# Kernel optimization log

Measured on AMD Instinct MI355X. Metric: run time of the kernel, lower is better.

The kernel has to match this reference:

```python
import jax, jax.numpy as jnp
import numpy as np

NA, NP = 50000, 100000  # num authors, num papers
NE = 200000             # edges per direction
H = 256


def _sage(x_src, x_dst, src, dst, Wl, bl, Wr, br, n_dst):
    # PyG SAGEConv: lin_l(mean_{j in N(i)} x_j) + lin_r(x_i)
    msg = x_src[src]                                              # [E, d_src] gather
    s = jax.ops.segment_sum(msg, dst, num_segments=n_dst)        # [n_dst, d_src]
    cnt = jax.ops.segment_sum(jnp.ones((src.shape[0],), x_src.dtype), dst, num_segments=n_dst)
    mean = s / jnp.maximum(cnt, 1.0)[:, None]
    return mean @ Wl.T + bl + x_dst @ Wr.T + br


def setup_inputs() -> dict:
    key = jax.random.key(0)
    ks = jax.random.split(key, 24)
    d = {}
    d['x_author'] = jax.random.normal(ks[0], (NA, 128), jnp.float32)
    d['x_paper'] = jax.random.normal(ks[1], (NP, 256), jnp.float32)
    src_a = jax.random.randint(ks[2], (NE,), 0, NA)
    dst_p = jax.random.randint(ks[3], (NE,), 0, NP)
    d['ei_a2p'] = jnp.stack([src_a, dst_p])                       # author -> paper
    src_p = jax.random.randint(ks[4], (NE,), 0, NP)
    dst_a = jax.random.randint(ks[5], (NE,), 0, NA)
    d['ei_p2a'] = jnp.stack([src_p, dst_a])                       # paper -> author
    sc = 0.05
    d['Wl0_ap'] = jax.random.normal(ks[6], (H, 128)) * sc
    d['bl0_ap'] = jnp.zeros((H,), jnp.float32)
    d['Wr0_ap'] = jax.random.normal(ks[7], (H, 256)) * sc
    d['br0_ap'] = jnp.zeros((H,), jnp.float32)
    d['Wl0_pa'] = jax.random.normal(ks[8], (H, 256)) * sc
    d['bl0_pa'] = jnp.zeros((H,), jnp.float32)
    d['Wr0_pa'] = jax.random.normal(ks[9], (H, 128)) * sc
    d['br0_pa'] = jnp.zeros((H,), jnp.float32)
    d['Wl_ap'] = jax.random.normal(ks[10], (2, H, H)) * sc
    d['bl_ap'] = jnp.zeros((2, H), jnp.float32)
    d['Wr_ap'] = jax.random.normal(ks[11], (2, H, H)) * sc
    d['br_ap'] = jnp.zeros((2, H), jnp.float32)
    d['Wl_pa'] = jax.random.normal(ks[12], (2, H, H)) * sc
    d['bl_pa'] = jnp.zeros((2, H), jnp.float32)
    d['Wr_pa'] = jax.random.normal(ks[13], (2, H, H)) * sc
    d['br_pa'] = jnp.zeros((2, H), jnp.float32)
    d['W_out'] = jax.random.normal(ks[14], (10, H)) * sc
    d['b_out'] = jnp.zeros((10,), jnp.float32)
    return d


def reference(x_author, x_paper, ei_a2p, ei_p2a,
              Wl0_ap, bl0_ap, Wr0_ap, br0_ap,
              Wl0_pa, bl0_pa, Wr0_pa, br0_pa,
              Wl_ap, bl_ap, Wr_ap, br_ap,
              Wl_pa, bl_pa, Wr_pa, br_pa,
              W_out, b_out):
    sa, da = ei_p2a[0], ei_p2a[1]   # paper->author edges
    sp, dp = ei_a2p[0], ei_a2p[1]   # author->paper edges
    # layer 0 (lazy dims: author 128, paper 256)
    paper = jax.nn.elu(_sage(x_author, x_paper, sp, dp, Wl0_ap, bl0_ap, Wr0_ap, br0_ap, NP))
    author = jax.nn.elu(_sage(x_paper, x_author, sa, da, Wl0_pa, bl0_pa, Wr0_pa, br0_pa, NA))
    # layers 1..2 (hidden 256)
    for l in range(2):
        new_paper = _sage(author, paper, sp, dp, Wl_ap[l], bl_ap[l], Wr_ap[l], br_ap[l], NP)
        new_author = _sage(paper, author, sa, da, Wl_pa[l], bl_pa[l], Wr_pa[l], br_pa[l], NA)
        paper = jax.nn.elu(new_paper)
        author = jax.nn.elu(new_author)
    return author @ W_out.T + b_out  # target = 'author'
```

## Files before the change

kernel.cpp:

```cpp
#include <hip/hip_runtime.h>
#include <hip/hip_bf16.h>
#include <cstddef>

#define NA 50000
#define NP 100000
#define NE 200000
#define SCAN_CHUNK 1024

typedef unsigned short u16;
typedef unsigned int u32;
typedef short v8s __attribute__((ext_vector_type(8)));
typedef float f32x4 __attribute__((ext_vector_type(4)));

__device__ __forceinline__ float elu_f(float x) {
  return x > 0.0f ? x : expm1f(x);
}
__device__ __forceinline__ u16 f2bf(float x) {
  u32 u = __float_as_uint(x);
  return (u16)((u + 0x7fffu + ((u >> 16) & 1u)) >> 16);
}
__device__ __forceinline__ float bf2f(u16 h) {
  return __uint_as_float(((u32)h) << 16);
}
__device__ __forceinline__ u32 pk2(float a, float b) {
  return (u32)f2bf(a) | ((u32)f2bf(b) << 16);
}
__device__ __forceinline__ float lo_f(u32 w) { return __uint_as_float(w << 16); }
__device__ __forceinline__ float hi_f(u32 w) { return __uint_as_float(w & 0xffff0000u); }

__device__ __forceinline__ void gload_lds16(const u16* gsrc, u16* ldst) {
  __builtin_amdgcn_global_load_lds(
      (const __attribute__((address_space(1))) u32*)gsrc,
      (__attribute__((address_space(3))) u32*)ldst, 16, 0, 0);
}

__global__ void count_deg_i(const int* __restrict__ dst_p, const int* __restrict__ dst_a,
                            int* cnt_p, int* cnt_a) {
  int i = blockIdx.x * blockDim.x + threadIdx.x;
  if (i < NE) atomicAdd(&cnt_p[dst_p[i]], 1);
  else if (i < 2 * NE) atomicAdd(&cnt_a[dst_a[i - NE]], 1);
}

__global__ void block_sums_k(const int* __restrict__ cnt, int* __restrict__ bsums, int n) {
  __shared__ int red[256];
  int t = threadIdx.x;
  int base = blockIdx.x * SCAN_CHUNK + t * 4;
  int s = 0;
  #pragma unroll
  for (int i = 0; i < 4; ++i) {
    int idx = base + i;
    if (idx < n) s += cnt[idx];
  }
  red[t] = s;
  __syncthreads();
  for (int off = 128; off > 0; off >>= 1) {
    if (t < off) red[t] += red[t + off];
    __syncthreads();
  }
  if (t == 0) bsums[blockIdx.x] = red[0];
}

__global__ void scan_bsums_k(int* bsums, int nb) {
  __shared__ int tmp[256];
  int t = threadIdx.x;
  int orig = (t < nb) ? bsums[t] : 0;
  tmp[t] = orig;
  __syncthreads();
  for (int off = 1; off < 256; off <<= 1) {
    int u = (t >= off) ? tmp[t - off] : 0;
    __syncthreads();
    tmp[t] += u;
    __syncthreads();
  }
  if (t < nb) bsums[t] = tmp[t] - orig;
}

__global__ void scan_final_k(const int* __restrict__ cnt, const int* __restrict__ bsums,
                             int* __restrict__ row_start, int* __restrict__ cursor,
                             int n, int total) {
  __shared__ int red[256];
  int t = threadIdx.x;
  int base = blockIdx.x * SCAN_CHUNK + t * 4;
  int v[4];
  int s = 0;
  #pragma unroll
  for (int i = 0; i < 4; ++i) {
    int idx = base + i;
    v[i] = (idx < n) ? cnt[idx] : 0;
    s += v[i];
  }
  int orig = s;
  red[t] = s;
  __syncthreads();
  for (int off = 1; off < 256; off <<= 1) {
    int u = (t >= off) ? red[t - off] : 0;
    __syncthreads();
    red[t] += u;
    __syncthreads();
  }
  int excl = red[t] - orig + bsums[blockIdx.x];
  #pragma unroll
  for (int i = 0; i < 4; ++i) {
    int idx = base + i;
    if (idx < n) {
      row_start[idx] = excl;
      cursor[idx] = excl;
    }
    excl += v[i];
  }
  if (blockIdx.x == 0 && t == 0) row_start[n] = total;
}

__global__ void csr_fill(const int* __restrict__ src, const int* __restrict__ dst,
                         int* cursor, int* __restrict__ csr_src) {
  int e = blockIdx.x * blockDim.x + threadIdx.x;
  if (e < NE) {
    int p = atomicAdd(&cursor[dst[e]], 1);
    csr_src[p] = src[e];
  }
}

__global__ void to_bf16(const float* __restrict__ in, u16* __restrict__ out, int n4) {
  int i = blockIdx.x * 256 + threadIdx.x;
  if (i >= n4) return;
  float4 v = ((const float4*)in)[i];
  uint2 o;
  o.x = pk2(v.x, v.y);
  o.y = pk2(v.z, v.w);
  *(uint2*)(out + (size_t)i * 4) = o;
}

struct PackJobs {
  const float* src[12];
  u16* dst[12];
  int K[12];
  int boff[13];
};

__global__ void pack_all(PackJobs J) {
  int blk = blockIdx.x;
  int j = 0;
  while (j < 11 && blk >= J.boff[j + 1]) ++j;
  int id = (blk - J.boff[j]) * 256 + threadIdx.x;
  int K = J.K[j];
  int l = id & 63;
  int c = (id >> 6) & 15;
  int ks = id >> 10;
  int n = c * 16 + (l & 15);
  int k = ks * 32 + (l >> 4) * 8;
  const float* src = J.src[j] + (size_t)n * K + k;
  uint4 o;
  o.x = pk2(src[0], src[1]);
  o.y = pk2(src[2], src[3]);
  o.z = pk2(src[4], src[5]);
  o.w = pk2(src[6], src[7]);
  *(uint4*)(J.dst[j] + (size_t)id * 8) = o;
}

struct BiasJobs {
  const float* a[6];
  const float* b[6];
  float* o[6];
};
__global__ void bias_all(BiasJobs J) {
  int j = blockIdx.x;
  int i = threadIdx.x;
  J.o[j][i] = J.a[j][i] + J.b[j][i];
}

template <int D>
__device__ __forceinline__ void gm_node(const u16* __restrict__ feat, const int* __restrict__ cs,
                                        const int* __restrict__ rs, u16* __restrict__ agg,
                                        int node, int lane) {
  int beg = rs[node], end = rs[node + 1];
  int deg = end - beg;
  if (D == 256) {
    float a0 = 0.f, a1 = 0.f, a2 = 0.f, a3 = 0.f, a4 = 0.f, a5 = 0.f, a6 = 0.f, a7 = 0.f;
    int e = beg;
    uint4 un = {0, 0, 0, 0};
    if (e < end) un = *(const uint4*)(feat + (size_t)cs[e] * 256 + lane * 8);
    while (e < end) {
      uint4 u = un;
      ++e;
      if (e < end)
        un = *(const uint4*)(feat + (size_t)cs[e] * 256 + lane * 8);
      a0 += lo_f(u.x); a1 += hi_f(u.x);
      a2 += lo_f(u.y); a3 += hi_f(u.y);
      a4 += lo_f(u.z); a5 += hi_f(u.z);
      a6 += lo_f(u.w); a7 += hi_f(u.w);
    }
    float inv = 1.0f / fmaxf((float)deg, 1.0f);
    uint4 o;
    o.x = pk2(a0 * inv, a1 * inv);
    o.y = pk2(a2 * inv, a3 * inv);
    o.z = pk2(a4 * inv, a5 * inv);
    o.w = pk2(a6 * inv, a7 * inv);
    *(uint4*)(agg + (size_t)node * 256 + lane * 8) = o;
  } else {
    float a0 = 0.f, a1 = 0.f, a2 = 0.f, a3 = 0.f;
    int e = beg;
    uint2 un = {0, 0};
    if (e < end) un = *(const uint2*)(feat + (size_t)cs[e] * 128 + lane * 4);
    while (e < end) {
      uint2 u = un;
      ++e;
      if (e < end)
        un = *(const uint2*)(feat + (size_t)cs[e] * 128 + lane * 4);
      a0 += lo_f(u.x); a1 += hi_f(u.x);
      a2 += lo_f(u.y); a3 += hi_f(u.y);
    }
    float inv = 1.0f / fmaxf((float)deg, 1.0f);
    uint2 o;
    o.x = pk2(a0 * inv, a1 * inv);
    o.y = pk2(a2 * inv, a3 * inv);
    *(uint2*)(agg + (size_t)node * 128 + lane * 4) = o;
  }
}

template <int D1, int D2>
__global__ __launch_bounds__(256) void gather2(
    const u16* __restrict__ f1, const int* __restrict__ cs1, const int* __restrict__ rs1,
    u16* __restrict__ a1, int n1,
    const u16* __restrict__ f2, const int* __restrict__ cs2, const int* __restrict__ rs2,
    u16* __restrict__ a2, int n2) {
  int hw = (blockIdx.x * 256 + threadIdx.x) >> 5;
  int lane = threadIdx.x & 31;
  if (hw < n1) gm_node<D1>(f1, cs1, rs1, a1, hw, lane);
  else if (hw - n1 < n2) gm_node<D2>(f2, cs2, rs2, a2, hw - n1, lane);
}

struct SideB {
  const u16* agg;
  const u16* x;
  const u16* Wp;
  const float* bias;
  u16* out;
  int M;
  int K1;
  int K2;
};

template <int NK>
__global__ __launch_bounds__(512, 4) void sage_pipe(SideB P, SideB A, int nbP2) {
  __shared__ __align__(16) u16 ldsw[3 * 4096];
  SideB S;
  int bid = blockIdx.x;
  if (bid < nbP2) { S = P; } else { bid -= nbP2; S = A; }
  const int cg = bid & 1;
  const int rg = bid >> 1;

  const int k1c = S.K1 >> 5;
  const int t = threadIdx.x;
  const int w = t >> 6, l = t & 63;
  const int lr = l & 15, lk = l >> 4;
  const int rowbase = rg * 256 + w * 32;

  int rowv[2];
  const u16 *pa[2], *px[2];
  #pragma unroll
  for (int rt = 0; rt < 2; ++rt) {
    int row = rowbase + rt * 16 + lr;
    rowv[rt] = row;
    int ar = min(row, S.M - 1);
    pa[rt] = S.agg + (size_t)ar * S.K1 + lk * 8;
    px[rt] = S.x + (size_t)ar * S.K2 + lk * 8;
  }

  auto xload = [&](int c, int rt) -> v8s {
    const u16* p = (c < k1c) ? (pa[rt] + c * 32) : (px[rt] + (c - k1c) * 32);
    return *(const v8s*)p;
  };
  auto wstage = [&](int c, int b) {
    const u16* gsrc = S.Wp + ((size_t)c * 1024 + cg * 512 + t) * 8;
    u16* ldst = ldsw + b * 4096 + w * 512;
    gload_lds16(gsrc, ldst);
  };

  f32x4 acc[2][8];
  #pragma unroll
  for (int rt = 0; rt < 2; ++rt)
    #pragma unroll
    for (int i = 0; i < 8; ++i) acc[rt][i] = (f32x4){0.f, 0.f, 0.f, 0.f};

  v8s xc[2], xn[2];
  xc[0] = xload(0, 0);
  xc[1] = xload(0, 1);
  wstage(0, 0);
  wstage(1, 1);
  asm volatile("s_waitcnt vmcnt(1)" ::: "memory");
  __builtin_amdgcn_s_barrier();

  #pragma unroll
  for (int s = 0; s < NK; ++s) {
    const int cur = s % 3;
    if (s + 2 < NK) wstage(s + 2, (s + 2) % 3);
    if (s + 1 < NK) {
      xn[0] = xload(s + 1, 0);
      xn[1] = xload(s + 1, 1);
    }
    const u16* lw = ldsw + cur * 4096 + (size_t)l * 8;
    #pragma unroll
    for (int i = 0; i < 8; ++i) {
      v8s wf = *(const v8s*)(lw + i * 512);
      acc[0][i] = __builtin_amdgcn_mfma_f32_16x16x32_bf16(wf, xc[0], acc[0][i], 0, 0, 0);
      acc[1][i] = __builtin_amdgcn_mfma_f32_16x16x32_bf16(wf, xc[1], acc[1][i], 0, 0, 0);
    }
    if (s + 1 < NK) {
      if (s + 2 < NK) {
        asm volatile("s_waitcnt vmcnt(3)" ::: "memory");
      } else {
        asm volatile("s_waitcnt vmcnt(2)" ::: "memory");
      }
      __builtin_amdgcn_s_barrier();
      xc[0] = xn[0];
      xc[1] = xn[1];
    }
  }

  const int colb = cg * 128 + lk * 4;
  #pragma unroll
  for (int rt = 0; rt < 2; ++rt) {
    if (rowv[rt] < S.M) {
      u16* orow = S.out + (size_t)rowv[rt] * 256 + colb;
      #pragma unroll
      for (int i = 0; i < 8; ++i) {
        f32x4 bv = *(const f32x4*)(S.bias + colb + i * 16);
        float e0 = elu_f(acc[rt][i][0] + bv[0]);
        float e1 = elu_f(acc[rt][i][1] + bv[1]);
        float e2 = elu_f(acc[rt][i][2] + bv[2]);
        float e3 = elu_f(acc[rt][i][3] + bv[3]);
        uint2 o;
        o.x = pk2(e0, e1);
        o.y = pk2(e2, e3);
        *(uint2*)(orow + i * 16) = o;
      }
    }
  }
}

__global__ __launch_bounds__(256) void out_proj(const u16* __restrict__ author,
                                                const float* __restrict__ W,
                                                const float* __restrict__ b,
                                                float* __restrict__ out, int M) {
  __shared__ float ws[10 * 256];
  __shared__ float bs[10];
  int t = threadIdx.x;
  for (int i = t; i < 2560; i += 256) ws[i] = W[i];
  if (t < 10) bs[t] = b[t];
  __syncthreads();
  int wave = t >> 6, lane = t & 63;
  int row = blockIdx.x * 4 + wave;
  if (row >= M) return;
  ushort4 u = *(const ushort4*)(author + (size_t)row * 256 + lane * 4);
  float a0 = bf2f(u.x), a1 = bf2f(u.y), a2 = bf2f(u.z), a3 = bf2f(u.w);
  float p[10];
  #pragma unroll
  for (int n = 0; n < 10; ++n) {
    const float* wv = ws + n * 256 + lane * 4;
    p[n] = a0 * wv[0] + a1 * wv[1] + a2 * wv[2] + a3 * wv[3];
  }
  #pragma unroll
  for (int off = 32; off > 0; off >>= 1) {
    #pragma unroll
    for (int n = 0; n < 10; ++n) p[n] += __shfl_down(p[n], off);
  }
  if (lane == 0) {
    #pragma unroll
    for (int n = 0; n < 10; ++n) out[(size_t)row * 10 + n] = p[n] + bs[n];
  }
}

extern "C" void kernel_launch(void* const* d_in, const int* in_sizes, int n_in,
                              void* d_out, int out_size, void* d_ws, size_t ws_size,
                              hipStream_t stream) {
  const float* x_author = (const float*)d_in[0];
  const float* x_paper  = (const float*)d_in[1];
  const int* ei_a2p = (const int*)d_in[2];
  const int* ei_p2a = (const int*)d_in[3];
  const int* src_ap = ei_a2p;
  const int* dst_ap = ei_a2p + NE;
  const int* src_pa = ei_p2a;
  const int* dst_pa = ei_p2a + NE;
  const float* Wl0_ap = (const float*)d_in[4];
  const float* bl0_ap = (const float*)d_in[5];
  const float* Wr0_ap = (const float*)d_in[6];
  const float* br0_ap = (const float*)d_in[7];
  const float* Wl0_pa = (const float*)d_in[8];
  const float* bl0_pa = (const float*)d_in[9];
  const float* Wr0_pa = (const float*)d_in[10];
  const float* br0_pa = (const float*)d_in[11];
  const float* Wl_ap = (const float*)d_in[12];
  const float* bl_ap = (const float*)d_in[13];
  const float* Wr_ap = (const float*)d_in[14];
  const float* br_ap = (const float*)d_in[15];
  const float* Wl_pa = (const float*)d_in[16];
  const float* bl_pa = (const float*)d_in[17];
  const float* Wr_pa = (const float*)d_in[18];
  const float* br_pa = (const float*)d_in[19];
  const float* W_out = (const float*)d_in[20];
  const float* b_out = (const float*)d_in[21];
  float* out = (float*)d_out;

  char* base = (char*)d_ws;
  size_t o = 0;
  auto alloc = [&](size_t bytes) {
    void* p = base + o;
    o += (bytes + 255) & ~(size_t)255;
    return p;
  };
  u16* paper   = (u16*)alloc((size_t)NP * 256 * 2);
  u16* author  = (u16*)alloc((size_t)NA * 256 * 2);
  u16* paper2  = (u16*)alloc((size_t)NP * 256 * 2);
  u16* author2 = (u16*)alloc((size_t)NA * 256 * 2);
  u16* agg_p  = (u16*)alloc((size_t)NP * 256 * 2);
  u16* agg_a  = (u16*)alloc((size_t)NA * 256 * 2);
  u16* xp_bf  = (u16*)alloc((size_t)NP * 256 * 2);
  u16* xa_bf  = (u16*)alloc((size_t)NA * 128 * 2);
  u16* wc0_p = (u16*)alloc((128 + 256) * 256 * 2);
  u16* wc0_a = (u16*)alloc((256 + 128) * 256 * 2);
  u16* wc_ap = (u16*)alloc((size_t)2 * 512 * 256 * 2);
  u16* wc_pa = (u16*)alloc((size_t)2 * 512 * 256 * 2);
  float* bias0_ap = (float*)alloc(256 * 4);
  float* bias0_pa = (float*)alloc(256 * 4);
  float* bias_ap  = (float*)alloc(2 * 256 * 4);
  float* bias_pa  = (float*)alloc(2 * 256 * 4);
  int* cnt_p  = (int*)alloc((size_t)(NP + NA) * 4);
  int* cnt_a  = cnt_p + NP;
  int* rs_p   = (int*)alloc((size_t)(NP + 1) * 4);
  int* rs_a   = (int*)alloc((size_t)(NA + 1) * 4);
  int* cur_p  = (int*)alloc((size_t)NP * 4);
  int* cur_a  = (int*)alloc((size_t)NA * 4);
  int* csrc_p = (int*)alloc((size_t)NE * 4);
  int* csrc_a = (int*)alloc((size_t)NE * 4);
  int* bsum_p = (int*)alloc(128 * 4);
  int* bsum_a = (int*)alloc(128 * 4);

  const int NBP = (NP + SCAN_CHUNK - 1) / SCAN_CHUNK;
  const int NBA = (NA + SCAN_CHUNK - 1) / SCAN_CHUNK;

  hipMemsetAsync(cnt_p, 0, (size_t)(NP + NA) * 4, stream);
  count_deg_i<<<(2 * NE + 255) / 256, 256, 0, stream>>>(dst_ap, dst_pa, cnt_p, cnt_a);
  block_sums_k<<<NBP, 256, 0, stream>>>(cnt_p, bsum_p, NP);
  block_sums_k<<<NBA, 256, 0, stream>>>(cnt_a, bsum_a, NA);
  scan_bsums_k<<<1, 256, 0, stream>>>(bsum_p, NBP);
  scan_bsums_k<<<1, 256, 0, stream>>>(bsum_a, NBA);
  scan_final_k<<<NBP, 256, 0, stream>>>(cnt_p, bsum_p, rs_p, cur_p, NP, NE);
  scan_final_k<<<NBA, 256, 0, stream>>>(cnt_a, bsum_a, rs_a, cur_a, NA, NE);
  csr_fill<<<(NE + 255) / 256, 256, 0, stream>>>(src_ap, dst_ap, cur_p, csrc_p);
  csr_fill<<<(NE + 255) / 256, 256, 0, stream>>>(src_pa, dst_pa, cur_a, csrc_a);

  to_bf16<<<((NP * 256 / 4) + 255) / 256, 256, 0, stream>>>(x_paper, xp_bf, NP * 256 / 4);
  to_bf16<<<((NA * 128 / 4) + 255) / 256, 256, 0, stream>>>(x_author, xa_bf, NA * 128 / 4);

  {
    PackJobs J;
    const float* srcs[12] = {Wl0_ap, Wr0_ap, Wl0_pa, Wr0_pa,
                             Wl_ap, Wr_ap, Wl_pa, Wr_pa,
                             Wl_ap + 65536, Wr_ap + 65536, Wl_pa + 65536, Wr_pa + 65536};
    u16* dsts[12] = {wc0_p, wc0_p + 128 * 256, wc0_a, wc0_a + 256 * 256,
                     wc_ap, wc_ap + 65536, wc_pa, wc_pa + 65536,
                     wc_ap + 131072, wc_ap + 131072 + 65536,
                     wc_pa + 131072, wc_pa + 131072 + 65536};
    int Ks[12] = {128, 256, 256, 128, 256, 256, 256, 256, 256, 256, 256, 256};
    int off = 0;
    for (int j = 0; j < 12; ++j) {
      J.src[j] = srcs[j];
      J.dst[j] = dsts[j];
      J.K[j] = Ks[j];
      J.boff[j] = off;
      off += Ks[j] / 8;
    }
    J.boff[12] = off;
    pack_all<<<off, 256, 0, stream>>>(J);
  }
  {
    BiasJobs J;
    const float* as[6] = {bl0_ap, bl0_pa, bl_ap, bl_ap + 256, bl_pa, bl_pa + 256};
    const float* bs[6] = {br0_ap, br0_pa, br_ap, br_ap + 256, br_pa, br_pa + 256};
    float* os[6] = {bias0_ap, bias0_pa, bias_ap, bias_ap + 256, bias_pa, bias_pa + 256};
    for (int j = 0; j < 6; ++j) { J.a[j] = as[j]; J.b[j] = bs[j]; J.o[j] = os[j]; }
    bias_all<<<6, 256, 0, stream>>>(J);
  }

  const int nbP2 = ((NP + 255) / 256) * 2;
  const int grid_sage = nbP2 + ((NA + 255) / 256) * 2;
  const int grid_gath = (NP + NA) / 8;

  gather2<128, 256><<<grid_gath, 256, 0, stream>>>(
      xa_bf, csrc_p, rs_p, agg_p, NP, xp_bf, csrc_a, rs_a, agg_a, NA);
  sage_pipe<12><<<grid_sage, 512, 0, stream>>>(
      SideB{agg_p, xp_bf, wc0_p, bias0_ap, paper, NP, 128, 256},
      SideB{agg_a, xa_bf, wc0_a, bias0_pa, author, NA, 256, 128}, nbP2);

  gather2<256, 256><<<grid_gath, 256, 0, stream>>>(
      author, csrc_p, rs_p, agg_p, NP, paper, csrc_a, rs_a, agg_a, NA);
  sage_pipe<16><<<grid_sage, 512, 0, stream>>>(
      SideB{agg_p, paper, wc_ap, bias_ap, paper2, NP, 256, 256},
      SideB{agg_a, author, wc_pa, bias_pa, author2, NA, 256, 256}, nbP2);

  gather2<256, 256><<<grid_gath, 256, 0, stream>>>(
      author2, csrc_p, rs_p, agg_p, NP, paper2, csrc_a, rs_a, agg_a, NA);
  sage_pipe<16><<<grid_sage, 512, 0, stream>>>(
      SideB{agg_p, paper2, wc_ap + 131072, bias_ap + 256, paper, NP, 256, 256},
      SideB{agg_a, author2, wc_pa + 131072, bias_pa + 256, author, NA, 256, 256}, nbP2);

  out_proj<<<(NA + 3) / 4, 256, 0, stream>>>(author, W_out, b_out, out, NA);
}
```

Measured before the change: 541.3 us.

## Fuse neighbor mean-gather into SAGE GEMM and skip unused last-layer paper update

The separate gather kernels that wrote mean-aggregated neighbor features to a workspace are removed. The SAGE GEMM kernel now computes each K-chunk of the aggregated row fragment in registers, directly from the CSR edge lists, before feeding it to the MFMA instructions. Tiles change to 128 rows by 256 columns with double-buffered weights in LDS. The final layer only computes the author side, because the paper output of that layer is never used. This removes the aggregate round trip through HBM and three launches, but the gather loads are no longer prefetched and stall the MFMA pipeline, and each block reloads its edge list once per K chunk.

```diff
diff --git a/kernel.cpp b/kernel.cpp
--- a/kernel.cpp
+++ b/kernel.cpp
@@ -11,6 +11,8 @@
 typedef unsigned int u32;
 typedef short v8s __attribute__((ext_vector_type(8)));
 typedef float f32x4 __attribute__((ext_vector_type(4)));
+
+union U8 { uint4 q; v8s v; };
 
 __device__ __forceinline__ float elu_f(float x) {
   return x > 0.0f ? x : expm1f(x);
@@ -168,69 +170,10 @@
   J.o[j][i] = J.a[j][i] + J.b[j][i];
 }
 
-template <int D>
-__device__ __forceinline__ void gm_node(const u16* __restrict__ feat, const int* __restrict__ cs,
-                                        const int* __restrict__ rs, u16* __restrict__ agg,
-                                        int node, int lane) {
-  int beg = rs[node], end = rs[node + 1];
-  int deg = end - beg;
-  if (D == 256) {
-    float a0 = 0.f, a1 = 0.f, a2 = 0.f, a3 = 0.f, a4 = 0.f, a5 = 0.f, a6 = 0.f, a7 = 0.f;
-    int e = beg;
-    uint4 un = {0, 0, 0, 0};
-    if (e < end) un = *(const uint4*)(feat + (size_t)cs[e] * 256 + lane * 8);
-    while (e < end) {
-      uint4 u = un;
-      ++e;
-      if (e < end)
-        un = *(const uint4*)(feat + (size_t)cs[e] * 256 + lane * 8);
-      a0 += lo_f(u.x); a1 += hi_f(u.x);
-      a2 += lo_f(u.y); a3 += hi_f(u.y);
-      a4 += lo_f(u.z); a5 += hi_f(u.z);
-      a6 += lo_f(u.w); a7 += hi_f(u.w);
-    }
-    float inv = 1.0f / fmaxf((float)deg, 1.0f);
-    uint4 o;
-    o.x = pk2(a0 * inv, a1 * inv);
-    o.y = pk2(a2 * inv, a3 * inv);
-    o.z = pk2(a4 * inv, a5 * inv);
-    o.w = pk2(a6 * inv, a7 * inv);
-    *(uint4*)(agg + (size_t)node * 256 + lane * 8) = o;
-  } else {
-    float a0 = 0.f, a1 = 0.f, a2 = 0.f, a3 = 0.f;
-    int e = beg;
-    uint2 un = {0, 0};
-    if (e < end) un = *(const uint2*)(feat + (size_t)cs[e] * 128 + lane * 4);
-    while (e < end) {
-      uint2 u = un;
-      ++e;
-      if (e < end)
-        un = *(const uint2*)(feat + (size_t)cs[e] * 128 + lane * 4);
-      a0 += lo_f(u.x); a1 += hi_f(u.x);
-      a2 += lo_f(u.y); a3 += hi_f(u.y);
-    }
-    float inv = 1.0f / fmaxf((float)deg, 1.0f);
-    uint2 o;
-    o.x = pk2(a0 * inv, a1 * inv);
-    o.y = pk2(a2 * inv, a3 * inv);
-    *(uint2*)(agg + (size_t)node * 128 + lane * 4) = o;
-  }
-}
-
-template <int D1, int D2>
-__global__ __launch_bounds__(256) void gather2(
-    const u16* __restrict__ f1, const int* __restrict__ cs1, const int* __restrict__ rs1,
-    u16* __restrict__ a1, int n1,
-    const u16* __restrict__ f2, const int* __restrict__ cs2, const int* __restrict__ rs2,
-    u16* __restrict__ a2, int n2) {
-  int hw = (blockIdx.x * 256 + threadIdx.x) >> 5;
-  int lane = threadIdx.x & 31;
-  if (hw < n1) gm_node<D1>(f1, cs1, rs1, a1, hw, lane);
-  else if (hw - n1 < n2) gm_node<D2>(f2, cs2, rs2, a2, hw - n1, lane);
-}
-
-struct SideB {
-  const u16* agg;
+struct SideF {
+  const u16* feat;
+  const int* cs;
+  const int* rs;
   const u16* x;
   const u16* Wp;
   const float* bias;
@@ -240,40 +183,52 @@
   int K2;
 };
 
-template <int NK>
-__global__ __launch_bounds__(512, 4) void sage_pipe(SideB P, SideB A, int nbP2) {
-  __shared__ __align__(16) u16 ldsw[3 * 4096];
-  SideB S;
+__global__ __launch_bounds__(512, 4) void sage_fgem(SideF P, SideF A, int nbP) {
+  __shared__ __align__(16) u16 ldsw[2][8192];
+  SideF S;
   int bid = blockIdx.x;
-  if (bid < nbP2) { S = P; } else { bid -= nbP2; S = A; }
-  const int cg = bid & 1;
-  const int rg = bid >> 1;
-
-  const int k1c = S.K1 >> 5;
+  if (bid < nbP) { S = P; } else { bid -= nbP; S = A; }
+
+  const int nk1 = S.K1 >> 5;
+  const int nk = nk1 + (S.K2 >> 5);
   const int t = threadIdx.x;
   const int w = t >> 6, l = t & 63;
+  const int rw = w & 3, cw = w >> 2;
   const int lr = l & 15, lk = l >> 4;
-  const int rowbase = rg * 256 + w * 32;
-
-  int rowv[2];
-  const u16 *pa[2], *px[2];
-  #pragma unroll
-  for (int rt = 0; rt < 2; ++rt) {
-    int row = rowbase + rt * 16 + lr;
-    rowv[rt] = row;
-    int ar = min(row, S.M - 1);
-    pa[rt] = S.agg + (size_t)ar * S.K1 + lk * 8;
-    px[rt] = S.x + (size_t)ar * S.K2 + lk * 8;
-  }
-
-  auto xload = [&](int c, int rt) -> v8s {
-    const u16* p = (c < k1c) ? (pa[rt] + c * 32) : (px[rt] + (c - k1c) * 32);
-    return *(const v8s*)p;
+  const int row0 = bid * 128 + rw * 32 + lr;
+  const int row1 = row0 + 16;
+  const int ar0 = min(row0, S.M - 1);
+  const int ar1 = min(row1, S.M - 1);
+  const int beg0 = S.rs[ar0], end0 = S.rs[ar0 + 1];
+  const int beg1 = S.rs[ar1], end1 = S.rs[ar1 + 1];
+  const float inv0 = 1.0f / fmaxf((float)(end0 - beg0), 1.0f);
+  const float inv1 = 1.0f / fmaxf((float)(end1 - beg1), 1.0f);
+  const u16* px0 = S.x + (size_t)ar0 * S.K2 + lk * 8;
+  const u16* px1 = S.x + (size_t)ar1 * S.K2 + lk * 8;
+
+  auto wstage = [&](int c, int b) {
+    const u16* g = S.Wp + (size_t)c * 8192 + (size_t)t * 8;
+    u16* d = ldsw[b] + w * 512;
+    gload_lds16(g, d);
+    gload_lds16(g + 4096, d + 4096);
   };
-  auto wstage = [&](int c, int b) {
-    const u16* gsrc = S.Wp + ((size_t)c * 1024 + cg * 512 + t) * 8;
-    u16* ldst = ldsw + b * 4096 + w * 512;
-    gload_lds16(gsrc, ldst);
+  auto gfrag = [&](int c, int beg, int end, float inv) -> v8s {
+    const u16* fb = S.feat + c * 32 + lk * 8;
+    float a0 = 0.f, a1 = 0.f, a2 = 0.f, a3 = 0.f;
+    float a4 = 0.f, a5 = 0.f, a6 = 0.f, a7 = 0.f;
+    for (int e = beg; e < end; ++e) {
+      uint4 u = *(const uint4*)(fb + (size_t)S.cs[e] * S.K1);
+      a0 += lo_f(u.x); a1 += hi_f(u.x);
+      a2 += lo_f(u.y); a3 += hi_f(u.y);
+      a4 += lo_f(u.z); a5 += hi_f(u.z);
+      a6 += lo_f(u.w); a7 += hi_f(u.w);
+    }
+    U8 r;
+    r.q.x = pk2(a0 * inv, a1 * inv);
+    r.q.y = pk2(a2 * inv, a3 * inv);
+    r.q.z = pk2(a4 * inv, a5 * inv);
+    r.q.w = pk2(a6 * inv, a7 * inv);
+    return r.v;
   };
 
   f32x4 acc[2][8];
@@ -282,46 +237,57 @@
     #pragma unroll
     for (int i = 0; i < 8; ++i) acc[rt][i] = (f32x4){0.f, 0.f, 0.f, 0.f};
 
-  v8s xc[2], xn[2];
-  xc[0] = xload(0, 0);
-  xc[1] = xload(0, 1);
   wstage(0, 0);
-  wstage(1, 1);
-  asm volatile("s_waitcnt vmcnt(1)" ::: "memory");
+  v8s xc0 = *(const v8s*)px0;
+  v8s xc1 = *(const v8s*)px1;
+  asm volatile("s_waitcnt vmcnt(0)" ::: "memory");
   __builtin_amdgcn_s_barrier();
 
-  #pragma unroll
-  for (int s = 0; s < NK; ++s) {
-    const int cur = s % 3;
-    if (s + 2 < NK) wstage(s + 2, (s + 2) % 3);
-    if (s + 1 < NK) {
-      xn[0] = xload(s + 1, 0);
-      xn[1] = xload(s + 1, 1);
-    }
-    const u16* lw = ldsw + cur * 4096 + (size_t)l * 8;
+  for (int c = 0; c < nk1; ++c) {
+    if (c + 1 < nk) wstage(c + 1, (c + 1) & 1);
+    v8s af0 = gfrag(c, beg0, end0, inv0);
+    v8s af1 = gfrag(c, beg1, end1, inv1);
+    const u16* lw = ldsw[c & 1] + cw * 4096 + (size_t)l * 8;
     #pragma unroll
     for (int i = 0; i < 8; ++i) {
       v8s wf = *(const v8s*)(lw + i * 512);
-      acc[0][i] = __builtin_amdgcn_mfma_f32_16x16x32_bf16(wf, xc[0], acc[0][i], 0, 0, 0);
-      acc[1][i] = __builtin_amdgcn_mfma_f32_16x16x32_bf16(wf, xc[1], acc[1][i], 0, 0, 0);
-    }
-    if (s + 1 < NK) {
-      if (s + 2 < NK) {
-        asm volatile("s_waitcnt vmcnt(3)" ::: "memory");
-      } else {
-        asm volatile("s_waitcnt vmcnt(2)" ::: "memory");
-      }
+      acc[0][i] = __builtin_amdgcn_mfma_f32_16x16x32_bf16(wf, af0, acc[0][i], 0, 0, 0);
+      acc[1][i] = __builtin_amdgcn_mfma_f32_16x16x32_bf16(wf, af1, acc[1][i], 0, 0, 0);
+    }
+    asm volatile("s_waitcnt vmcnt(0)" ::: "memory");
+    __builtin_amdgcn_s_barrier();
+  }
+
+  for (int c = nk1; c < nk; ++c) {
+    const bool more = (c + 1 < nk);
+    v8s xn0, xn1;
+    if (more) {
+      wstage(c + 1, (c + 1) & 1);
+      const int off = (c + 1 - nk1) * 32;
+      xn0 = *(const v8s*)(px0 + off);
+      xn1 = *(const v8s*)(px1 + off);
+    }
+    const u16* lw = ldsw[c & 1] + cw * 4096 + (size_t)l * 8;
+    #pragma unroll
+    for (int i = 0; i < 8; ++i) {
+      v8s wf = *(const v8s*)(lw + i * 512);
+      acc[0][i] = __builtin_amdgcn_mfma_f32_16x16x32_bf16(wf, xc0, acc[0][i], 0, 0, 0);
+      acc[1][i] = __builtin_amdgcn_mfma_f32_16x16x32_bf16(wf, xc1, acc[1][i], 0, 0, 0);
+    }
+    if (more) {
+      asm volatile("s_waitcnt vmcnt(2)" ::: "memory");
       __builtin_amdgcn_s_barrier();
-      xc[0] = xn[0];
-      xc[1] = xn[1];
-    }
-  }
-
-  const int colb = cg * 128 + lk * 4;
+      xc0 = xn0;
+      xc1 = xn1;
+    }
+  }
+
+  const int colb = cw * 128 + lk * 4;
   #pragma unroll
   for (int rt = 0; rt < 2; ++rt) {
-    if (rowv[rt] < S.M) {
-      u16* orow = S.out + (size_t)rowv[rt] * 256 + colb;
+    const int row = rt == 0 ? row0 : row1;
+    if (row < S.M) {
+      u16* orow = S.out + (size_t)row * 256 + colb;
       #pragma unroll
       for (int i = 0; i < 8; ++i) {
         f32x4 bv = *(const f32x4*)(S.bias + colb + i * 16);
@@ -412,8 +378,6 @@
   u16* author  = (u16*)alloc((size_t)NA * 256 * 2);
   u16* paper2  = (u16*)alloc((size_t)NP * 256 * 2);
   u16* author2 = (u16*)alloc((size_t)NA * 256 * 2);
-  u16* agg_p  = (u16*)alloc((size_t)NP * 256 * 2);
-  u16* agg_a  = (u16*)alloc((size_t)NA * 256 * 2);
   u16* xp_bf  = (u16*)alloc((size_t)NP * 256 * 2);
   u16* xa_bf  = (u16*)alloc((size_t)NA * 128 * 2);
   u16* wc0_p = (u16*)alloc((128 + 256) * 256 * 2);
@@ -482,27 +446,20 @@
     bias_all<<<6, 256, 0, stream>>>(J);
   }
 
-  const int nbP2 = ((NP + 255) / 256) * 2;
-  const int grid_sage = nbP2 + ((NA + 255) / 256) * 2;
-  const int grid_gath = (NP + NA) / 8;
-
-  gather2<128, 256><<<grid_gath, 256, 0, stream>>>(
-      xa_bf, csrc_p, rs_p, agg_p, NP, xp_bf, csrc_a, rs_a, agg_a, NA);
-  sage_pipe<12><<<grid_sage, 512, 0, stream>>>(
-      SideB{agg_p, xp_bf, wc0_p, bias0_ap, paper, NP, 128, 256},
-      SideB{agg_a, xa_bf, wc0_a, bias0_pa, author, NA, 256, 128}, nbP2);
-
-  gather2<256, 256><<<grid_gath, 256, 0, stream>>>(
-      author, csrc_p, rs_p, agg_p, NP, paper, csrc_a, rs_a, agg_a, NA);
-  sage_pipe<16><<<grid_sage, 512, 0, stream>>>(
-      SideB{agg_p, paper, wc_ap, bias_ap, paper2, NP, 256, 256},
-      SideB{agg_a, author, wc_pa, bias_pa, author2, NA, 256, 256}, nbP2);
-
-  gather2<256, 256><<<grid_gath, 256, 0, stream>>>(
-      author2, csrc_p, rs_p, agg_p, NP, paper2, csrc_a, rs_a, agg_a, NA);
-  sage_pipe<16><<<grid_sage, 512, 0, stream>>>(
-      SideB{agg_p, paper2, wc_ap + 131072, bias_ap + 256, paper, NP, 256, 256},
-      SideB{agg_a, author2, wc_pa + 131072, bias_pa + 256, author, NA, 256, 256}, nbP2);
+  const int nbP = (NP + 127) / 128;
+  const int nbA = (NA + 127) / 128;
+
+  sage_fgem<<<nbP + nbA, 512, 0, stream>>>(
+      SideF{xa_bf, csrc_p, rs_p, xp_bf, wc0_p, bias0_ap, paper, NP, 128, 256},
+      SideF{xp_bf, csrc_a, rs_a, xa_bf, wc0_a, bias0_pa, author, NA, 256, 128}, nbP);
+
+  sage_fgem<<<nbP + nbA, 512, 0, stream>>>(
+      SideF{author, csrc_p, rs_p, paper, wc_ap, bias_ap, paper2, NP, 256, 256},
+      SideF{paper, csrc_a, rs_a, author, wc_pa, bias_pa, author2, NA, 256, 256}, nbP);
+
+  sage_fgem<<<nbA, 512, 0, stream>>>(
+      SideF{paper2, csrc_a, rs_a, author2, wc_pa + 131072, bias_pa + 256, author, NA, 256, 256},
+      SideF{paper2, csrc_a, rs_a, author2, wc_pa + 131072, bias_pa + 256, author, NA, 256, 256}, 0);
 
   out_proj<<<(NA + 3) / 4, 256, 0, stream>>>(author, W_out, b_out, out, NA);
 }
```

Result: slower. 711.1 us (+31.4%).
